# Optimization experiments

Measured on AMD Instinct MI355X. Metric: run time of the kernel, lower is better.

## Reference

```python
import jax, jax.numpy as jnp
import numpy as np

D_MODEL, D_STATE, EXPAND = 1024, 256, 2
BATCH, SEQ = 8, 2048


def setup_inputs() -> dict:
    key = jax.random.key(0)
    ks = jax.random.split(key, 7)
    s = 0.02
    return {
        "x": jax.random.normal(ks[0], (BATCH, SEQ, D_MODEL), jnp.float32),
        "W_in": jax.random.normal(ks[1], (D_MODEL, D_MODEL * EXPAND), jnp.float32) * s,
        "b_in": jax.random.normal(ks[2], (D_MODEL * EXPAND,), jnp.float32) * s,
        "W_state": jax.random.normal(ks[3], (D_MODEL * EXPAND, D_STATE), jnp.float32) * s,
        "b_state": jax.random.normal(ks[4], (D_STATE,), jnp.float32) * s,
        "W_out": jax.random.normal(ks[5], (D_STATE, D_MODEL), jnp.float32) * s,
        "b_out": jax.random.normal(ks[6], (D_MODEL,), jnp.float32) * s,
        "init_state": jnp.zeros((1, D_STATE), jnp.float32),
    }


def reference(x, W_in, b_in, W_state, b_state, W_out, b_out, init_state):
    # x: [B, T, D]
    x_proj = jax.nn.silu(jnp.einsum("btd,de->bte", x, W_in) + b_in)  # [B,T,2D]
    # state_proj depends only on x_proj, so batch the GEMM over all timesteps
    updates = jnp.einsum("bte,es->bts", x_proj, W_state) + b_state    # [B,T,S]
    updates_t = jnp.swapaxes(updates, 0, 1)                            # [T,B,S]
    state0 = jnp.broadcast_to(init_state, (x.shape[0], init_state.shape[1]))

    def step(state, u):
        new = jax.nn.silu(state + u)
        return new, new

    _, states = jax.lax.scan(step, state0, updates_t)  # [T,B,S]
    out = jnp.einsum("tbs,sd->tbd", states, W_out) + b_out  # [T,B,D]
    return jnp.swapaxes(out, 0, 1)  # [B,T,D]
```

## Files before the change

kernel.cpp:

```cpp
#include <hip/hip_runtime.h>
#include <cstdint>
#include <cstddef>

#define BATCH 8
#define SEQ   2048
#define DM    1024
#define DE    2048
#define DSZ   256
#define MROWS (BATCH*SEQ)
#define MCHUNK 8192

typedef _Float16 f16;
typedef _Float16 f16x4 __attribute__((ext_vector_type(4)));
typedef _Float16 f16x8 __attribute__((ext_vector_type(8)));
typedef float  f32x4  __attribute__((ext_vector_type(4)));

__device__ __forceinline__ void glds16(const void* gp, void* lp) {
  __builtin_amdgcn_global_load_lds(
      (const __attribute__((address_space(1))) void*)gp,
      (__attribute__((address_space(3))) void*)lp, 16, 0, 0);
}

__device__ __forceinline__ float silu_f(float x) {
  return x * __builtin_amdgcn_rcpf(1.0f + __expf(-x));
}

__device__ __forceinline__ int swz(int k8, int r) { return k8 ^ ((r >> 1) & 3); }

__global__ void split_x_k(const float* __restrict__ in, f16* __restrict__ oh,
                          f16* __restrict__ ol, int n) {
  int i = (blockIdx.x * blockDim.x + threadIdx.x) * 4;
  const int stride = gridDim.x * blockDim.x * 4;
  for (; i < n; i += stride) {
    float4 v = *(const float4*)(in + i);
    f16x4 h, l;
    h[0] = (f16)v.x; l[0] = (f16)(v.x - (float)h[0]);
    h[1] = (f16)v.y; l[1] = (f16)(v.y - (float)h[1]);
    h[2] = (f16)v.z; l[2] = (f16)(v.z - (float)h[2]);
    h[3] = (f16)v.w; l[3] = (f16)(v.w - (float)h[3]);
    *(f16x4*)(oh + i) = h;
    *(f16x4*)(ol + i) = l;
  }
}

__global__ void transpose_split_k(const float* __restrict__ in, f16* __restrict__ oh,
                                  f16* __restrict__ ol, int R, int C) {
  __shared__ float tile[32][33];
  const int c0 = blockIdx.x * 32, r0 = blockIdx.y * 32;
  const int tx = threadIdx.x, ty = threadIdx.y;
  #pragma unroll
  for (int i = 0; i < 4; ++i)
    tile[ty + i*8][tx] = in[(size_t)(r0 + ty + i*8) * C + c0 + tx];
  __syncthreads();
  #pragma unroll
  for (int i = 0; i < 4; ++i) {
    float v = tile[tx][ty + i*8];
    f16 h = (f16)v;
    size_t idx = (size_t)(c0 + ty + i*8) * R + r0 + tx;
    oh[idx] = h;
    ol[idx] = (f16)(v - (float)h);
  }
}

__global__ void transpose_cast_f16_k(const float* __restrict__ in, f16* __restrict__ out, int R, int C) {
  __shared__ float tile[32][33];
  const int c0 = blockIdx.x * 32, r0 = blockIdx.y * 32;
  const int tx = threadIdx.x, ty = threadIdx.y;
  #pragma unroll
  for (int i = 0; i < 4; ++i)
    tile[ty + i*8][tx] = in[(size_t)(r0 + ty + i*8) * C + c0 + tx];
  __syncthreads();
  #pragma unroll
  for (int i = 0; i < 4; ++i)
    out[(size_t)(c0 + ty + i*8) * R + r0 + tx] = (f16)tile[tx][ty + i*8];
}

__global__ __launch_bounds__(512) void gemm1_k(const f16* __restrict__ Ah, const f16* __restrict__ Al,
                                               const f16* __restrict__ Bh, const f16* __restrict__ Bl,
                                               const float* __restrict__ bias,
                                               f16* __restrict__ Ch, f16* __restrict__ Cl) {
  const int K = 1024, N = 2048;
  __shared__ f16 sAh[4096], sAl[4096], sBh[4096], sBl[4096];

  const int tid = threadIdx.x;
  const int w = tid >> 6, l = tid & 63;
  const int bid = blockIdx.x;
  const int xcd = bid & 7, loc = bid >> 3;
  const int mt = xcd * 8 + (loc & 7);
  const int nt = loc >> 3;
  const int bm = mt * 128, bn = nt * 128;
  const int wm = (w >> 2) * 64, wn = (w & 3) * 32;
  const int lr = l & 15, lq = l >> 4;

  const int r = tid >> 2, k8 = swz(tid & 3, r);
  const f16* pAh = Ah + (size_t)(bm + r) * K + k8 * 8;
  const f16* pAl = Al + (size_t)(bm + r) * K + k8 * 8;
  const f16* pBh = Bh + (size_t)(bn + r) * K + k8 * 8;
  const f16* pBl = Bl + (size_t)(bn + r) * K + k8 * 8;
  f16* dAh = sAh + tid * 8; f16* dAl = sAl + tid * 8;
  f16* dBh = sBh + tid * 8; f16* dBl = sBl + tid * 8;

  int offA[4], offB[2];
  #pragma unroll
  for (int i = 0; i < 4; ++i) {
    const int row = wm + i*16 + lr;
    offA[i] = row * 32 + swz(lq, row) * 8;
  }
  #pragma unroll
  for (int j = 0; j < 2; ++j) {
    const int row = wn + j*16 + lr;
    offB[j] = row * 32 + swz(lq, row) * 8;
  }

  f32x4 acc[4][2] = {};

  for (int kk = 0; kk < K; kk += 32) {
    __syncthreads();
    glds16(pAh, dAh); glds16(pAl, dAl);
    glds16(pBh, dBh); glds16(pBl, dBl);
    pAh += 32; pAl += 32; pBh += 32; pBl += 32;
    asm volatile("s_waitcnt vmcnt(0)" ::: "memory");
    __syncthreads();

    f16x8 ah[4], al[4], bh[2], bl[2];
    #pragma unroll
    for (int i = 0; i < 4; ++i) {
      ah[i] = *(const f16x8*)(sAh + offA[i]);
      al[i] = *(const f16x8*)(sAl + offA[i]);
    }
    #pragma unroll
    for (int j = 0; j < 2; ++j) {
      bh[j] = *(const f16x8*)(sBh + offB[j]);
      bl[j] = *(const f16x8*)(sBl + offB[j]);
    }
    #pragma unroll
    for (int i = 0; i < 4; ++i)
      #pragma unroll
      for (int j = 0; j < 2; ++j) {
        acc[i][j] = __builtin_amdgcn_mfma_f32_16x16x32_f16(ah[i], bh[j], acc[i][j], 0, 0, 0);
        acc[i][j] = __builtin_amdgcn_mfma_f32_16x16x32_f16(ah[i], bl[j], acc[i][j], 0, 0, 0);
        acc[i][j] = __builtin_amdgcn_mfma_f32_16x16x32_f16(al[i], bh[j], acc[i][j], 0, 0, 0);
      }
  }

  #pragma unroll
  for (int j = 0; j < 2; ++j) {
    const int col = bn + wn + j*16 + lr;
    const float bv = bias[col];
    #pragma unroll
    for (int i = 0; i < 4; ++i)
      #pragma unroll
      for (int r4 = 0; r4 < 4; ++r4) {
        const int row = bm + wm + i*16 + lq*4 + r4;
        const float s = silu_f(acc[i][j][r4] + bv);
        const f16 h = (f16)s;
        const size_t idx = (size_t)row * N + col;
        Ch[idx] = h;
        Cl[idx] = (f16)(s - (float)h);
      }
  }
}

__global__ __launch_bounds__(256) void gemm2s_k(const f16* __restrict__ Ah, const f16* __restrict__ Al,
                                                const f16* __restrict__ Bh, const f16* __restrict__ Bl,
                                                const float* __restrict__ bias,
                                                float* __restrict__ C) {
  const int K = 2048, N = 256;
  __shared__ f16 sAh[2048], sAl[2048], sBh[2048], sBl[2048];

  const int tid = threadIdx.x;
  const int w = tid >> 6, l = tid & 63;
  const int bm = blockIdx.y * 64, bn = blockIdx.x * 64;
  const int wm = (w & 1) * 32, wn = (w >> 1) * 32;
  const int lr = l & 15, lq = l >> 4;

  const int r = tid >> 2, k8 = swz(tid & 3, r);
  const f16* pAh = Ah + (size_t)(bm + r) * K + k8 * 8;
  const f16* pAl = Al + (size_t)(bm + r) * K + k8 * 8;
  const f16* pBh = Bh + (size_t)(bn + r) * K + k8 * 8;
  const f16* pBl = Bl + (size_t)(bn + r) * K + k8 * 8;
  f16* dAh = sAh + tid * 8; f16* dAl = sAl + tid * 8;
  f16* dBh = sBh + tid * 8; f16* dBl = sBl + tid * 8;

  int offA[2], offB[2];
  #pragma unroll
  for (int i = 0; i < 2; ++i) {
    const int row = wm + i*16 + lr;
    offA[i] = row * 32 + swz(lq, row) * 8;
  }
  #pragma unroll
  for (int j = 0; j < 2; ++j) {
    const int row = wn + j*16 + lr;
    offB[j] = row * 32 + swz(lq, row) * 8;
  }

  f32x4 acc[2][2] = {};

  for (int kk = 0; kk < K; kk += 32) {
    __syncthreads();
    glds16(pAh, dAh); glds16(pAl, dAl);
    glds16(pBh, dBh); glds16(pBl, dBl);
    pAh += 32; pAl += 32; pBh += 32; pBl += 32;
    asm volatile("s_waitcnt vmcnt(0)" ::: "memory");
    __syncthreads();

    f16x8 ah[2], al[2], bh[2], bl[2];
    #pragma unroll
    for (int i = 0; i < 2; ++i) {
      ah[i] = *(const f16x8*)(sAh + offA[i]);
      al[i] = *(const f16x8*)(sAl + offA[i]);
    }
    #pragma unroll
    for (int j = 0; j < 2; ++j) {
      bh[j] = *(const f16x8*)(sBh + offB[j]);
      bl[j] = *(const f16x8*)(sBl + offB[j]);
    }
    #pragma unroll
    for (int i = 0; i < 2; ++i)
      #pragma unroll
      for (int j = 0; j < 2; ++j) {
        acc[i][j] = __builtin_amdgcn_mfma_f32_16x16x32_f16(ah[i], bh[j], acc[i][j], 0, 0, 0);
        acc[i][j] = __builtin_amdgcn_mfma_f32_16x16x32_f16(ah[i], bl[j], acc[i][j], 0, 0, 0);
        acc[i][j] = __builtin_amdgcn_mfma_f32_16x16x32_f16(al[i], bh[j], acc[i][j], 0, 0, 0);
      }
  }

  #pragma unroll
  for (int j = 0; j < 2; ++j) {
    const int col = bn + wn + j*16 + lr;
    const float bv = bias[col];
    #pragma unroll
    for (int i = 0; i < 2; ++i)
      #pragma unroll
      for (int r4 = 0; r4 < 4; ++r4) {
        const int row = bm + wm + i*16 + lq*4 + r4;
        C[(size_t)row * N + col] = acc[i][j][r4] + bv;
      }
  }
}

__global__ __launch_bounds__(256) void gemm3_k(const f16* __restrict__ A,
                                               const f16* __restrict__ Bt,
                                               const float* __restrict__ bias,
                                               float* __restrict__ C) {
  const int K = 256, N = 1024;
  __shared__ f16 sA[4096], sB[4096];

  const int tid = threadIdx.x;
  const int w = tid >> 6, l = tid & 63;
  const int bm = blockIdx.y * 128, bn = blockIdx.x * 128;
  const int wm = (w >> 1) * 64, wn = (w & 1) * 64;
  const int lr = l & 15, lq = l >> 4;

  const f16 *pA[2], *pB[2]; f16 *dA[2], *dB[2];
  #pragma unroll
  for (int p = 0; p < 2; ++p) {
    const int c = p * 256 + tid;
    const int r = c >> 2, k8 = swz(c & 3, r);
    pA[p] = A  + (size_t)(bm + r) * K + k8 * 8;
    pB[p] = Bt + (size_t)(bn + r) * K + k8 * 8;
    dA[p] = sA + (size_t)c * 8;
    dB[p] = sB + (size_t)c * 8;
  }

  int offA[4], offB[4];
  #pragma unroll
  for (int i = 0; i < 4; ++i) {
    const int rowA = wm + i*16 + lr;
    const int rowB = wn + i*16 + lr;
    offA[i] = rowA * 32 + swz(lq, rowA) * 8;
    offB[i] = rowB * 32 + swz(lq, rowB) * 8;
  }

  f32x4 acc[4][4] = {};

  for (int kk = 0; kk < K; kk += 32) {
    __syncthreads();
    glds16(pA[0], dA[0]); glds16(pA[1], dA[1]);
    glds16(pB[0], dB[0]); glds16(pB[1], dB[1]);
    pA[0] += 32; pA[1] += 32; pB[0] += 32; pB[1] += 32;
    asm volatile("s_waitcnt vmcnt(0)" ::: "memory");
    __syncthreads();

    f16x8 af[4], bfr[4];
    #pragma unroll
    for (int i = 0; i < 4; ++i) af[i]  = *(const f16x8*)(sA + offA[i]);
    #pragma unroll
    for (int j = 0; j < 4; ++j) bfr[j] = *(const f16x8*)(sB + offB[j]);
    #pragma unroll
    for (int i = 0; i < 4; ++i)
      #pragma unroll
      for (int j = 0; j < 4; ++j)
        acc[i][j] = __builtin_amdgcn_mfma_f32_16x16x32_f16(af[i], bfr[j], acc[i][j], 0, 0, 0);
  }

  #pragma unroll
  for (int j = 0; j < 4; ++j) {
    const int col = bn + wn + j*16 + lr;
    const float bv = bias[col];
    #pragma unroll
    for (int i = 0; i < 4; ++i)
      #pragma unroll
      for (int r4 = 0; r4 < 4; ++r4) {
        const int row = bm + wm + i*16 + lq*4 + r4;
        C[(size_t)row * N + col] = acc[i][j][r4] + bv;
      }
  }
}

#define L2E 1.4426950408889634f
__global__ __launch_bounds__(64) void scan_k(const float* __restrict__ upd,
                                             const float* __restrict__ init,
                                             f16* __restrict__ states) {
  const int b = blockIdx.x >> 2, sq = blockIdx.x & 3;
  const int s = sq * 64 + threadIdx.x;
  const float* u = upd + (size_t)b * SEQ * DSZ + s;
  f16* st = states + (size_t)b * SEQ * DSZ + s;
  float state = init[s];

  float r0[16], r1[16], r2[16], ulog[16];
  #pragma unroll
  for (int i = 0; i < 16; ++i) r0[i] = u[(size_t)i * DSZ];
  #pragma unroll
  for (int i = 0; i < 16; ++i) r1[i] = u[(size_t)(16 + i) * DSZ];
  #pragma unroll
  for (int i = 0; i < 16; ++i) ulog[i] = r0[i] * (-L2E);

  for (int t0 = 0; t0 < SEQ; t0 += 16) {
    if (t0 + 32 < SEQ) {
      #pragma unroll
      for (int i = 0; i < 16; ++i) r2[i] = u[(size_t)(t0 + 32 + i) * DSZ];
    }
    f16 res[16];
    #pragma unroll
    for (int i = 0; i < 16; ++i) {
      const float e = __builtin_amdgcn_exp2f(__builtin_fmaf(state, -L2E, ulog[i]));
      const float x = state + r0[i];
      state = x * __builtin_amdgcn_rcpf(1.0f + e);
      res[i] = (f16)state;
    }
    #pragma unroll
    for (int i = 0; i < 16; ++i) st[(size_t)(t0 + i) * DSZ] = res[i];
    #pragma unroll
    for (int i = 0; i < 16; ++i) { r0[i] = r1[i]; ulog[i] = r1[i] * (-L2E); r1[i] = r2[i]; }
  }
}

extern "C" void kernel_launch(void* const* d_in, const int* in_sizes, int n_in,
                              void* d_out, int out_size, void* d_ws, size_t ws_size,
                              hipStream_t stream) {
  const float* x       = (const float*)d_in[0];
  const float* W_in    = (const float*)d_in[1];
  const float* b_in    = (const float*)d_in[2];
  const float* W_state = (const float*)d_in[3];
  const float* b_state = (const float*)d_in[4];
  const float* W_out   = (const float*)d_in[5];
  const float* b_out   = (const float*)d_in[6];
  const float* init_st = (const float*)d_in[7];
  float* out = (float*)d_out;

  char* ws = (char*)d_ws;
  f16*   xh        = (f16*)(ws + 0);
  f16*   xl        = (f16*)(ws + 33554432);
  f16*   xproj_h   = (f16*)(ws + 67108864);
  f16*   xproj_l   = (f16*)(ws + 100663296);
  float* upd       = (float*)(ws + 134217728);
  f16*   states    = (f16*)(ws + 150994944);
  f16*   w_in_h    = (f16*)(ws + 159383552);
  f16*   w_in_l    = (f16*)(ws + 163577856);
  f16*   w_state_h = (f16*)(ws + 167772160);
  f16*   w_state_l = (f16*)(ws + 168820736);
  f16*   w_out_t   = (f16*)(ws + 169869312);

  split_x_k<<<4096, 256, 0, stream>>>(x, xh, xl, MROWS * DM);
  dim3 tb(32, 8);
  transpose_split_k<<<dim3(DE/32,  DM/32), tb, 0, stream>>>(W_in,    w_in_h,    w_in_l,    DM,  DE);
  transpose_split_k<<<dim3(DSZ/32, DE/32), tb, 0, stream>>>(W_state, w_state_h, w_state_l, DE,  DSZ);
  transpose_cast_f16_k<<<dim3(DM/32, DSZ/32), tb, 0, stream>>>(W_out, w_out_t, DSZ, DM);

  for (int c = 0; c < 2; ++c) {
    const size_t ro = (size_t)c * MCHUNK;
    gemm1_k<<<1024, 512, 0, stream>>>(
        xh + ro * DM, xl + ro * DM, w_in_h, w_in_l, b_in, xproj_h, xproj_l);
    gemm2s_k<<<dim3(DSZ/64, MCHUNK/64), 256, 0, stream>>>(
        xproj_h, xproj_l, w_state_h, w_state_l, b_state, upd + ro * DSZ);
  }

  scan_k<<<BATCH*4, 64, 0, stream>>>(upd, init_st, states);

  gemm3_k<<<dim3(DM/128, MROWS/128), 256, 0, stream>>>(states, w_out_t, b_out, out);
}
```

Measured before the change: 577.7 us.

## Split-K the state projection GEMM with atomic accumulation, move bias into scan

The state-projection GEMM now splits its K=2048 reduction into four 512-wide slices across a third grid dimension and accumulates partial results into a pre-zeroed buffer with float atomicAdd. The aim is more parallelism than the original 512 blocks per chunk and shorter per-block K loops. The bias add moves into the scan kernel, and the scan's prefetch pipeline is deepened by one extra 16-step register buffer. The cost is an extra zeroing pass, atomic traffic on the output, and a sum order that is no longer deterministic.

```diff
diff --git a/kernel.cpp b/kernel.cpp
--- a/kernel.cpp
+++ b/kernel.cpp
@@ -75,6 +75,13 @@
     out[(size_t)(c0 + ty + i*8) * R + r0 + tx] = (f16)tile[tx][ty + i*8];
 }
 
+__global__ void zero_k(float* __restrict__ p, int n) {
+  int i = (blockIdx.x * blockDim.x + threadIdx.x) * 4;
+  const int stride = gridDim.x * blockDim.x * 4;
+  for (; i < n; i += stride)
+    *(float4*)(p + i) = make_float4(0.f, 0.f, 0.f, 0.f);
+}
+
 __global__ __launch_bounds__(512) void gemm1_k(const f16* __restrict__ Ah, const f16* __restrict__ Al,
                                                const f16* __restrict__ Bh, const f16* __restrict__ Bl,
                                                const float* __restrict__ bias,
@@ -161,24 +168,24 @@
   }
 }
 
-__global__ __launch_bounds__(256) void gemm2s_k(const f16* __restrict__ Ah, const f16* __restrict__ Al,
-                                                const f16* __restrict__ Bh, const f16* __restrict__ Bl,
-                                                const float* __restrict__ bias,
-                                                float* __restrict__ C) {
-  const int K = 2048, N = 256;
+__global__ __launch_bounds__(256) void gemm2sk_k(const f16* __restrict__ Ah, const f16* __restrict__ Al,
+                                                 const f16* __restrict__ Bh, const f16* __restrict__ Bl,
+                                                 float* __restrict__ C) {
+  const int K = 2048, N = 256, KSPL = 512;
   __shared__ f16 sAh[2048], sAl[2048], sBh[2048], sBl[2048];
 
   const int tid = threadIdx.x;
   const int w = tid >> 6, l = tid & 63;
   const int bm = blockIdx.y * 64, bn = blockIdx.x * 64;
+  const int k0 = blockIdx.z * KSPL;
   const int wm = (w & 1) * 32, wn = (w >> 1) * 32;
   const int lr = l & 15, lq = l >> 4;
 
   const int r = tid >> 2, k8 = swz(tid & 3, r);
-  const f16* pAh = Ah + (size_t)(bm + r) * K + k8 * 8;
-  const f16* pAl = Al + (size_t)(bm + r) * K + k8 * 8;
-  const f16* pBh = Bh + (size_t)(bn + r) * K + k8 * 8;
-  const f16* pBl = Bl + (size_t)(bn + r) * K + k8 * 8;
+  const f16* pAh = Ah + (size_t)(bm + r) * K + k0 + k8 * 8;
+  const f16* pAl = Al + (size_t)(bm + r) * K + k0 + k8 * 8;
+  const f16* pBh = Bh + (size_t)(bn + r) * K + k0 + k8 * 8;
+  const f16* pBl = Bl + (size_t)(bn + r) * K + k0 + k8 * 8;
   f16* dAh = sAh + tid * 8; f16* dAl = sAl + tid * 8;
   f16* dBh = sBh + tid * 8; f16* dBl = sBl + tid * 8;
 
@@ -196,7 +203,7 @@
 
   f32x4 acc[2][2] = {};
 
-  for (int kk = 0; kk < K; kk += 32) {
+  for (int kk = 0; kk < KSPL; kk += 32) {
     __syncthreads();
     glds16(pAh, dAh); glds16(pAl, dAl);
     glds16(pBh, dBh); glds16(pBl, dBl);
@@ -228,13 +235,12 @@
   #pragma unroll
   for (int j = 0; j < 2; ++j) {
     const int col = bn + wn + j*16 + lr;
-    const float bv = bias[col];
     #pragma unroll
     for (int i = 0; i < 2; ++i)
       #pragma unroll
       for (int r4 = 0; r4 < 4; ++r4) {
         const int row = bm + wm + i*16 + lq*4 + r4;
-        C[(size_t)row * N + col] = acc[i][j][r4] + bv;
+        atomicAdd(&C[(size_t)row * N + col], acc[i][j][r4]);
       }
   }
 }
@@ -311,25 +317,29 @@
 #define L2E 1.4426950408889634f
 __global__ __launch_bounds__(64) void scan_k(const float* __restrict__ upd,
                                              const float* __restrict__ init,
+                                             const float* __restrict__ b_state,
                                              f16* __restrict__ states) {
   const int b = blockIdx.x >> 2, sq = blockIdx.x & 3;
   const int s = sq * 64 + threadIdx.x;
+  const float bs = b_state[s];
   const float* u = upd + (size_t)b * SEQ * DSZ + s;
   f16* st = states + (size_t)b * SEQ * DSZ + s;
   float state = init[s];
 
-  float r0[16], r1[16], r2[16], ulog[16];
-  #pragma unroll
-  for (int i = 0; i < 16; ++i) r0[i] = u[(size_t)i * DSZ];
+  float r0[16], r1[16], r2[16], r3[16], ulog[16];
+  #pragma unroll
+  for (int i = 0; i < 16; ++i) r0[i] = u[(size_t)i * DSZ] + bs;
   #pragma unroll
   for (int i = 0; i < 16; ++i) r1[i] = u[(size_t)(16 + i) * DSZ];
   #pragma unroll
+  for (int i = 0; i < 16; ++i) r2[i] = u[(size_t)(32 + i) * DSZ];
+  #pragma unroll
   for (int i = 0; i < 16; ++i) ulog[i] = r0[i] * (-L2E);
 
   for (int t0 = 0; t0 < SEQ; t0 += 16) {
-    if (t0 + 32 < SEQ) {
-      #pragma unroll
-      for (int i = 0; i < 16; ++i) r2[i] = u[(size_t)(t0 + 32 + i) * DSZ];
+    if (t0 + 48 < SEQ) {
+      #pragma unroll
+      for (int i = 0; i < 16; ++i) r3[i] = u[(size_t)(t0 + 48 + i) * DSZ];
     }
     f16 res[16];
     #pragma unroll
@@ -342,7 +352,10 @@
     #pragma unroll
     for (int i = 0; i < 16; ++i) st[(size_t)(t0 + i) * DSZ] = res[i];
     #pragma unroll
-    for (int i = 0; i < 16; ++i) { r0[i] = r1[i]; ulog[i] = r1[i] * (-L2E); r1[i] = r2[i]; }
+    for (int i = 0; i < 16; ++i) {
+      r0[i] = r1[i] + bs; ulog[i] = r0[i] * (-L2E);
+      r1[i] = r2[i]; r2[i] = r3[i];
+    }
   }
 }
 
@@ -377,16 +390,17 @@
   transpose_split_k<<<dim3(DE/32,  DM/32), tb, 0, stream>>>(W_in,    w_in_h,    w_in_l,    DM,  DE);
   transpose_split_k<<<dim3(DSZ/32, DE/32), tb, 0, stream>>>(W_state, w_state_h, w_state_l, DE,  DSZ);
   transpose_cast_f16_k<<<dim3(DM/32, DSZ/32), tb, 0, stream>>>(W_out, w_out_t, DSZ, DM);
+  zero_k<<<1024, 256, 0, stream>>>(upd, MROWS * DSZ);
 
   for (int c = 0; c < 2; ++c) {
     const size_t ro = (size_t)c * MCHUNK;
     gemm1_k<<<1024, 512, 0, stream>>>(
         xh + ro * DM, xl + ro * DM, w_in_h, w_in_l, b_in, xproj_h, xproj_l);
-    gemm2s_k<<<dim3(DSZ/64, MCHUNK/64), 256, 0, stream>>>(
-        xproj_h, xproj_l, w_state_h, w_state_l, b_state, upd + ro * DSZ);
-  }
-
-  scan_k<<<BATCH*4, 64, 0, stream>>>(upd, init_st, states);
+    gemm2sk_k<<<dim3(DSZ/64, MCHUNK/64, 4), 256, 0, stream>>>(
+        xproj_h, xproj_l, w_state_h, w_state_l, upd + ro * DSZ);
+  }
+
+  scan_k<<<BATCH*4, 64, 0, stream>>>(upd, init_st, b_state, states);
 
   gemm3_k<<<dim3(DM/128, MROWS/128), 256, 0, stream>>>(states, w_out_t, b_out, out);
 }
```

Result: slower. 593.2 us (+2.7%).

## Restructure gemm1 into 4-stage async LDS pipeline with 256 threads and 64x64 warp tiles

Applied to the files above, without the earlier changes.

Rewrites the first GEMM to stream the three split-precision products (hi*hi, hi*lo, lo*hi) as 96 sequential k-tiles, one operand pair per tile, through a 4-slot LDS ring buffer. Loads run two tiles ahead with partial vmcnt waits and a single barrier per tile, so global-to-LDS transfers overlap with MFMA work. The block shrinks to 256 threads, each warp covers a 64x64 tile, and MFMA sections run at raised s_setprio. In exchange there is more register pressure per thread from the 16 accumulators. With one barrier per stage, reusing slots four deep depends on the prefetch distance of two to stay race-free.

```diff
diff --git a/kernel.cpp b/kernel.cpp
--- a/kernel.cpp
+++ b/kernel.cpp
@@ -75,12 +75,12 @@
     out[(size_t)(c0 + ty + i*8) * R + r0 + tx] = (f16)tile[tx][ty + i*8];
 }
 
-__global__ __launch_bounds__(512) void gemm1_k(const f16* __restrict__ Ah, const f16* __restrict__ Al,
+__global__ __launch_bounds__(256) void gemm1_k(const f16* __restrict__ Ah, const f16* __restrict__ Al,
                                                const f16* __restrict__ Bh, const f16* __restrict__ Bl,
                                                const float* __restrict__ bias,
                                                f16* __restrict__ Ch, f16* __restrict__ Cl) {
   const int K = 1024, N = 2048;
-  __shared__ f16 sAh[4096], sAl[4096], sBh[4096], sBl[4096];
+  __shared__ f16 sA[16384], sB[16384];
 
   const int tid = threadIdx.x;
   const int w = tid >> 6, l = tid & 63;
@@ -89,62 +89,76 @@
   const int mt = xcd * 8 + (loc & 7);
   const int nt = loc >> 3;
   const int bm = mt * 128, bn = nt * 128;
-  const int wm = (w >> 2) * 64, wn = (w & 3) * 32;
+  const int wm = (w >> 1) * 64, wn = (w & 1) * 64;
   const int lr = l & 15, lq = l >> 4;
 
-  const int r = tid >> 2, k8 = swz(tid & 3, r);
-  const f16* pAh = Ah + (size_t)(bm + r) * K + k8 * 8;
-  const f16* pAl = Al + (size_t)(bm + r) * K + k8 * 8;
-  const f16* pBh = Bh + (size_t)(bn + r) * K + k8 * 8;
-  const f16* pBl = Bl + (size_t)(bn + r) * K + k8 * 8;
-  f16* dAh = sAh + tid * 8; f16* dAl = sAl + tid * 8;
-  f16* dBh = sBh + tid * 8; f16* dBl = sBl + tid * 8;
-
-  int offA[4], offB[2];
+  int aoff[2], gdst[2];
+  #pragma unroll
+  for (int p = 0; p < 2; ++p) {
+    const int g = p * 256 + tid;
+    const int r = g >> 2, k8 = swz(g & 3, r);
+    aoff[p] = r * K + k8 * 8;
+    gdst[p] = g * 8;
+  }
+
+  int offA[4], offB[4];
   #pragma unroll
   for (int i = 0; i < 4; ++i) {
-    const int row = wm + i*16 + lr;
-    offA[i] = row * 32 + swz(lq, row) * 8;
-  }
-  #pragma unroll
-  for (int j = 0; j < 2; ++j) {
-    const int row = wn + j*16 + lr;
-    offB[j] = row * 32 + swz(lq, row) * 8;
-  }
-
-  f32x4 acc[4][2] = {};
-
-  for (int kk = 0; kk < K; kk += 32) {
-    __syncthreads();
-    glds16(pAh, dAh); glds16(pAl, dAl);
-    glds16(pBh, dBh); glds16(pBl, dBl);
-    pAh += 32; pAl += 32; pBh += 32; pBl += 32;
-    asm volatile("s_waitcnt vmcnt(0)" ::: "memory");
-    __syncthreads();
-
-    f16x8 ah[4], al[4], bh[2], bl[2];
-    #pragma unroll
-    for (int i = 0; i < 4; ++i) {
-      ah[i] = *(const f16x8*)(sAh + offA[i]);
-      al[i] = *(const f16x8*)(sAl + offA[i]);
-    }
-    #pragma unroll
-    for (int j = 0; j < 2; ++j) {
-      bh[j] = *(const f16x8*)(sBh + offB[j]);
-      bl[j] = *(const f16x8*)(sBl + offB[j]);
-    }
+    const int rowA = wm + i*16 + lr;
+    const int rowB = wn + i*16 + lr;
+    offA[i] = rowA * 32 + swz(lq, rowA) * 8;
+    offB[i] = rowB * 32 + swz(lq, rowB) * 8;
+  }
+
+  const f16* Abm_h = Ah + (size_t)bm * K;
+  const f16* Abm_l = Al + (size_t)bm * K;
+  const f16* Bbn_h = Bh + (size_t)bn * K;
+  const f16* Bbn_l = Bl + (size_t)bn * K;
+
+  auto stage = [&](int kt) {
+    const int s = kt & 3, seg = kt >> 5, koff = (kt & 31) * 32;
+    const f16* Ab = (seg < 2 ? Abm_h : Abm_l) + koff;
+    const f16* Bb = (seg == 1 ? Bbn_l : Bbn_h) + koff;
+    f16* dA = sA + s * 4096;
+    f16* dB = sB + s * 4096;
+    glds16(Ab + aoff[0], dA + gdst[0]);
+    glds16(Ab + aoff[1], dA + gdst[1]);
+    glds16(Bb + aoff[0], dB + gdst[0]);
+    glds16(Bb + aoff[1], dB + gdst[1]);
+  };
+
+  f32x4 acc[4][4] = {};
+
+  stage(0);
+  stage(1);
+
+  for (int kt = 0; kt < 96; ++kt) {
+    if (kt < 94) stage(kt + 2);
+    if (kt < 94)       asm volatile("s_waitcnt vmcnt(8)" ::: "memory");
+    else if (kt == 94) asm volatile("s_waitcnt vmcnt(4)" ::: "memory");
+    else               asm volatile("s_waitcnt vmcnt(0)" ::: "memory");
+    __builtin_amdgcn_s_barrier();
+    asm volatile("" ::: "memory");
+
+    const int s = kt & 3;
+    const f16* bA = sA + s * 4096;
+    const f16* bB = sB + s * 4096;
+    f16x8 af[4], bfr[4];
+    #pragma unroll
+    for (int i = 0; i < 4; ++i) af[i]  = *(const f16x8*)(bA + offA[i]);
+    #pragma unroll
+    for (int j = 0; j < 4; ++j) bfr[j] = *(const f16x8*)(bB + offB[j]);
+    __builtin_amdgcn_s_setprio(1);
     #pragma unroll
     for (int i = 0; i < 4; ++i)
       #pragma unroll
-      for (int j = 0; j < 2; ++j) {
-        acc[i][j] = __builtin_amdgcn_mfma_f32_16x16x32_f16(ah[i], bh[j], acc[i][j], 0, 0, 0);
-        acc[i][j] = __builtin_amdgcn_mfma_f32_16x16x32_f16(ah[i], bl[j], acc[i][j], 0, 0, 0);
-        acc[i][j] = __builtin_amdgcn_mfma_f32_16x16x32_f16(al[i], bh[j], acc[i][j], 0, 0, 0);
-      }
-  }
-
-  #pragma unroll
-  for (int j = 0; j < 2; ++j) {
+      for (int j = 0; j < 4; ++j)
+        acc[i][j] = __builtin_amdgcn_mfma_f32_16x16x32_f16(af[i], bfr[j], acc[i][j], 0, 0, 0);
+    __builtin_amdgcn_s_setprio(0);
+  }
+
+  #pragma unroll
+  for (int j = 0; j < 4; ++j) {
     const int col = bn + wn + j*16 + lr;
     const float bv = bias[col];
     #pragma unroll
@@ -152,11 +166,11 @@
       #pragma unroll
       for (int r4 = 0; r4 < 4; ++r4) {
         const int row = bm + wm + i*16 + lq*4 + r4;
-        const float s = silu_f(acc[i][j][r4] + bv);
-        const f16 h = (f16)s;
+        const float sv = silu_f(acc[i][j][r4] + bv);
+        const f16 h = (f16)sv;
         const size_t idx = (size_t)row * N + col;
         Ch[idx] = h;
-        Cl[idx] = (f16)(s - (float)h);
+        Cl[idx] = (f16)(sv - (float)h);
       }
   }
 }
@@ -380,7 +394,7 @@
 
   for (int c = 0; c < 2; ++c) {
     const size_t ro = (size_t)c * MCHUNK;
-    gemm1_k<<<1024, 512, 0, stream>>>(
+    gemm1_k<<<1024, 256, 0, stream>>>(
         xh + ro * DM, xl + ro * DM, w_in_h, w_in_l, b_in, xproj_h, xproj_l);
     gemm2s_k<<<dim3(DSZ/64, MCHUNK/64), 256, 0, stream>>>(
         xproj_h, xproj_l, w_state_h, w_state_l, b_state, upd + ro * DSZ);
```

Result: slower. 615.0 us (+6.4%).

## Double-buffer LDS tiles in all three GEMMs to overlap loads with MFMA

Applied to the files above, without the earlier changes.

Each GEMM kernel now keeps two LDS buffers. It issues the global-to-LDS DMA for the next K tile before running the MFMAs on the current one, so there is one barrier per iteration instead of two, and the explicit vmcnt(0) wait is gone. Wave priority is also raised around the MFMA block with s_setprio. This is meant to hide global load latency behind compute. The cost is doubled LDS use, which may lower occupancy, and correctness now depends on the barrier ordering the async LDS writes correctly, since the explicit wait was removed.

```diff
diff --git a/kernel.cpp b/kernel.cpp
--- a/kernel.cpp
+++ b/kernel.cpp
@@ -80,7 +80,7 @@
                                                const float* __restrict__ bias,
                                                f16* __restrict__ Ch, f16* __restrict__ Cl) {
   const int K = 1024, N = 2048;
-  __shared__ f16 sAh[4096], sAl[4096], sBh[4096], sBl[4096];
+  __shared__ f16 sAh[2][4096], sAl[2][4096], sBh[2][4096], sBl[2][4096];
 
   const int tid = threadIdx.x;
   const int w = tid >> 6, l = tid & 63;
@@ -97,8 +97,7 @@
   const f16* pAl = Al + (size_t)(bm + r) * K + k8 * 8;
   const f16* pBh = Bh + (size_t)(bn + r) * K + k8 * 8;
   const f16* pBl = Bl + (size_t)(bn + r) * K + k8 * 8;
-  f16* dAh = sAh + tid * 8; f16* dAl = sAl + tid * 8;
-  f16* dBh = sBh + tid * 8; f16* dBl = sBl + tid * 8;
+  const int dst = tid * 8;
 
   int offA[4], offB[2];
   #pragma unroll
@@ -114,25 +113,31 @@
 
   f32x4 acc[4][2] = {};
 
-  for (int kk = 0; kk < K; kk += 32) {
-    __syncthreads();
-    glds16(pAh, dAh); glds16(pAl, dAl);
-    glds16(pBh, dBh); glds16(pBl, dBl);
-    pAh += 32; pAl += 32; pBh += 32; pBl += 32;
-    asm volatile("s_waitcnt vmcnt(0)" ::: "memory");
-    __syncthreads();
-
+  glds16(pAh, &sAh[0][dst]); glds16(pAl, &sAl[0][dst]);
+  glds16(pBh, &sBh[0][dst]); glds16(pBl, &sBl[0][dst]);
+  pAh += 32; pAl += 32; pBh += 32; pBl += 32;
+  __syncthreads();
+
+  for (int kt = 0; kt < 32; ++kt) {
+    const int cur = kt & 1;
+    if (kt < 31) {
+      const int nxt = cur ^ 1;
+      glds16(pAh, &sAh[nxt][dst]); glds16(pAl, &sAl[nxt][dst]);
+      glds16(pBh, &sBh[nxt][dst]); glds16(pBl, &sBl[nxt][dst]);
+      pAh += 32; pAl += 32; pBh += 32; pBl += 32;
+    }
     f16x8 ah[4], al[4], bh[2], bl[2];
     #pragma unroll
     for (int i = 0; i < 4; ++i) {
-      ah[i] = *(const f16x8*)(sAh + offA[i]);
-      al[i] = *(const f16x8*)(sAl + offA[i]);
+      ah[i] = *(const f16x8*)(&sAh[cur][0] + offA[i]);
+      al[i] = *(const f16x8*)(&sAl[cur][0] + offA[i]);
     }
     #pragma unroll
     for (int j = 0; j < 2; ++j) {
-      bh[j] = *(const f16x8*)(sBh + offB[j]);
-      bl[j] = *(const f16x8*)(sBl + offB[j]);
-    }
+      bh[j] = *(const f16x8*)(&sBh[cur][0] + offB[j]);
+      bl[j] = *(const f16x8*)(&sBl[cur][0] + offB[j]);
+    }
+    __builtin_amdgcn_s_setprio(1);
     #pragma unroll
     for (int i = 0; i < 4; ++i)
       #pragma unroll
@@ -141,6 +146,8 @@
         acc[i][j] = __builtin_amdgcn_mfma_f32_16x16x32_f16(ah[i], bl[j], acc[i][j], 0, 0, 0);
         acc[i][j] = __builtin_amdgcn_mfma_f32_16x16x32_f16(al[i], bh[j], acc[i][j], 0, 0, 0);
       }
+    __builtin_amdgcn_s_setprio(0);
+    __syncthreads();
   }
 
   #pragma unroll
@@ -166,7 +173,7 @@
                                                 const float* __restrict__ bias,
                                                 float* __restrict__ C) {
   const int K = 2048, N = 256;
-  __shared__ f16 sAh[2048], sAl[2048], sBh[2048], sBl[2048];
+  __shared__ f16 sAh[2][2048], sAl[2][2048], sBh[2][2048], sBl[2][2048];
 
   const int tid = threadIdx.x;
   const int w = tid >> 6, l = tid & 63;
@@ -179,8 +186,7 @@
   const f16* pAl = Al + (size_t)(bm + r) * K + k8 * 8;
   const f16* pBh = Bh + (size_t)(bn + r) * K + k8 * 8;
   const f16* pBl = Bl + (size_t)(bn + r) * K + k8 * 8;
-  f16* dAh = sAh + tid * 8; f16* dAl = sAl + tid * 8;
-  f16* dBh = sBh + tid * 8; f16* dBl = sBl + tid * 8;
+  const int dst = tid * 8;
 
   int offA[2], offB[2];
   #pragma unroll
@@ -196,25 +202,31 @@
 
   f32x4 acc[2][2] = {};
 
-  for (int kk = 0; kk < K; kk += 32) {
-    __syncthreads();
-    glds16(pAh, dAh); glds16(pAl, dAl);
-    glds16(pBh, dBh); glds16(pBl, dBl);
-    pAh += 32; pAl += 32; pBh += 32; pBl += 32;
-    asm volatile("s_waitcnt vmcnt(0)" ::: "memory");
-    __syncthreads();
-
+  glds16(pAh, &sAh[0][dst]); glds16(pAl, &sAl[0][dst]);
+  glds16(pBh, &sBh[0][dst]); glds16(pBl, &sBl[0][dst]);
+  pAh += 32; pAl += 32; pBh += 32; pBl += 32;
+  __syncthreads();
+
+  for (int kt = 0; kt < 64; ++kt) {
+    const int cur = kt & 1;
+    if (kt < 63) {
+      const int nxt = cur ^ 1;
+      glds16(pAh, &sAh[nxt][dst]); glds16(pAl, &sAl[nxt][dst]);
+      glds16(pBh, &sBh[nxt][dst]); glds16(pBl, &sBl[nxt][dst]);
+      pAh += 32; pAl += 32; pBh += 32; pBl += 32;
+    }
     f16x8 ah[2], al[2], bh[2], bl[2];
     #pragma unroll
     for (int i = 0; i < 2; ++i) {
-      ah[i] = *(const f16x8*)(sAh + offA[i]);
-      al[i] = *(const f16x8*)(sAl + offA[i]);
+      ah[i] = *(const f16x8*)(&sAh[cur][0] + offA[i]);
+      al[i] = *(const f16x8*)(&sAl[cur][0] + offA[i]);
     }
     #pragma unroll
     for (int j = 0; j < 2; ++j) {
-      bh[j] = *(const f16x8*)(sBh + offB[j]);
-      bl[j] = *(const f16x8*)(sBl + offB[j]);
-    }
+      bh[j] = *(const f16x8*)(&sBh[cur][0] + offB[j]);
+      bl[j] = *(const f16x8*)(&sBl[cur][0] + offB[j]);
+    }
+    __builtin_amdgcn_s_setprio(1);
     #pragma unroll
     for (int i = 0; i < 2; ++i)
       #pragma unroll
@@ -223,6 +235,8 @@
         acc[i][j] = __builtin_amdgcn_mfma_f32_16x16x32_f16(ah[i], bl[j], acc[i][j], 0, 0, 0);
         acc[i][j] = __builtin_amdgcn_mfma_f32_16x16x32_f16(al[i], bh[j], acc[i][j], 0, 0, 0);
       }
+    __builtin_amdgcn_s_setprio(0);
+    __syncthreads();
   }
 
   #pragma unroll
@@ -244,7 +258,7 @@
                                                const float* __restrict__ bias,
                                                float* __restrict__ C) {
   const int K = 256, N = 1024;
-  __shared__ f16 sA[4096], sB[4096];
+  __shared__ f16 sA[2][4096], sB[2][4096];
 
   const int tid = threadIdx.x;
   const int w = tid >> 6, l = tid & 63;
@@ -252,15 +266,14 @@
   const int wm = (w >> 1) * 64, wn = (w & 1) * 64;
   const int lr = l & 15, lq = l >> 4;
 
-  const f16 *pA[2], *pB[2]; f16 *dA[2], *dB[2];
+  const f16 *pA[2], *pB[2]; int dstc[2];
   #pragma unroll
   for (int p = 0; p < 2; ++p) {
     const int c = p * 256 + tid;
     const int r = c >> 2, k8 = swz(c & 3, r);
     pA[p] = A  + (size_t)(bm + r) * K + k8 * 8;
     pB[p] = Bt + (size_t)(bn + r) * K + k8 * 8;
-    dA[p] = sA + (size_t)c * 8;
-    dB[p] = sB + (size_t)c * 8;
+    dstc[p] = c * 8;
   }
 
   int offA[4], offB[4];
@@ -274,24 +287,32 @@
 
   f32x4 acc[4][4] = {};
 
-  for (int kk = 0; kk < K; kk += 32) {
-    __syncthreads();
-    glds16(pA[0], dA[0]); glds16(pA[1], dA[1]);
-    glds16(pB[0], dB[0]); glds16(pB[1], dB[1]);
-    pA[0] += 32; pA[1] += 32; pB[0] += 32; pB[1] += 32;
-    asm volatile("s_waitcnt vmcnt(0)" ::: "memory");
-    __syncthreads();
-
+  glds16(pA[0], &sA[0][dstc[0]]); glds16(pA[1], &sA[0][dstc[1]]);
+  glds16(pB[0], &sB[0][dstc[0]]); glds16(pB[1], &sB[0][dstc[1]]);
+  pA[0] += 32; pA[1] += 32; pB[0] += 32; pB[1] += 32;
+  __syncthreads();
+
+  for (int kt = 0; kt < 8; ++kt) {
+    const int cur = kt & 1;
+    if (kt < 7) {
+      const int nxt = cur ^ 1;
+      glds16(pA[0], &sA[nxt][dstc[0]]); glds16(pA[1], &sA[nxt][dstc[1]]);
+      glds16(pB[0], &sB[nxt][dstc[0]]); glds16(pB[1], &sB[nxt][dstc[1]]);
+      pA[0] += 32; pA[1] += 32; pB[0] += 32; pB[1] += 32;
+    }
     f16x8 af[4], bfr[4];
     #pragma unroll
-    for (int i = 0; i < 4; ++i) af[i]  = *(const f16x8*)(sA + offA[i]);
-    #pragma unroll
-    for (int j = 0; j < 4; ++j) bfr[j] = *(const f16x8*)(sB + offB[j]);
+    for (int i = 0; i < 4; ++i) af[i]  = *(const f16x8*)(&sA[cur][0] + offA[i]);
+    #pragma unroll
+    for (int j = 0; j < 4; ++j) bfr[j] = *(const f16x8*)(&sB[cur][0] + offB[j]);
+    __builtin_amdgcn_s_setprio(1);
     #pragma unroll
     for (int i = 0; i < 4; ++i)
       #pragma unroll
       for (int j = 0; j < 4; ++j)
         acc[i][j] = __builtin_amdgcn_mfma_f32_16x16x32_f16(af[i], bfr[j], acc[i][j], 0, 0, 0);
+    __builtin_amdgcn_s_setprio(0);
+    __syncthreads();
   }
 
   #pragma unroll
```

New measurement: 563.6 us. -2.5%, faster.
